# Performance work log

Hardware: AMD Instinct MI355X
Metric: run time of the kernel (lower is better)

## Reference

```python
import jax, jax.numpy as jnp
import numpy as np

BS, T, SIDE, H, Z, NSPK = 2048, 34, 30, 128, 16, 1024


def _lrelu(x):
    # nn.LeakyReLU(True) -> negative_slope=1.0, i.e. identity (faithful to source)
    return x


def _gru_cell(x, h, wih, whh, bih, bhh):
    # PyTorch GRU cell, gate order (r, z, n)
    gi = x @ wih.T + bih
    gh = h @ whh.T + bhh
    ir, iz, inn = jnp.split(gi, 3, axis=-1)
    hr, hz, hn = jnp.split(gh, 3, axis=-1)
    r = jax.nn.sigmoid(ir + hr)
    z = jax.nn.sigmoid(iz + hz)
    n = jnp.tanh(inn + r * hn)
    return (1.0 - z) * n + z * h


def setup_inputs() -> dict:
    key = jax.random.key(0)
    ks = iter(jax.random.split(key, 64))
    rn = lambda shape, s=0.05: jax.random.normal(next(ks), shape, jnp.float32) * s
    inp = {}
    inp["pre_seq"] = jax.random.normal(next(ks), (BS, T, 28), jnp.float32)
    inp["beats"] = jax.random.normal(next(ks), (BS, 2, T * SIDE), jnp.float32)
    inp["in_text"] = jnp.zeros((BS, T), jnp.int32)   # unused by forward
    inp["in_audio"] = jnp.zeros((BS, 1), jnp.float32)  # unused by forward
    inp["vid_indices"] = jax.random.randint(next(ks), (BS,), 0, NSPK)
    inp["eps"] = jax.random.normal(next(ks), (BS, Z), jnp.float32)  # reparameterize noise
    # speaker embedding net
    inp["spk_table"] = rn((NSPK, Z))
    inp["spk_lin_w"] = rn((Z, Z)); inp["spk_lin_b"] = jnp.zeros((Z,))
    inp["mu_w"] = rn((Z, Z)); inp["mu_b"] = jnp.zeros((Z,))
    inp["lv_w"] = rn((Z, Z)); inp["lv_b"] = jnp.zeros((Z,))
    # per-step MLPs
    inp["squ_w"] = rn((H, 3 * SIDE)); inp["squ_b"] = jnp.zeros((H,))
    inp["oenv_w"] = rn((H, 3 * SIDE)); inp["oenv_b"] = jnp.zeros((H,))
    inp["pose_w"] = rn((16, 28)); inp["pose_b"] = jnp.zeros((16,))
    inp["out_w"] = rn((H, H + 16)); inp["out_b"] = jnp.zeros((H,))
    inp["bo_w1"] = rn((64, H)); inp["bo_b1"] = jnp.zeros((64,))
    inp["bo_w2"] = rn((27, 64)); inp["bo_b2"] = jnp.zeros((27,))
    # GRU: 4 layers, bidirectional, hidden 128; layer0 input 144, layers1-3 input 256
    inp["w_ih_l0"] = rn((2, 3 * H, H + 16)); inp["w_hh_l0"] = rn((2, 3 * H, H))
    inp["b_ih_l0"] = jnp.zeros((2, 3 * H)); inp["b_hh_l0"] = jnp.zeros((2, 3 * H))
    inp["w_ih"] = rn((3, 2, 3 * H, 2 * H)); inp["w_hh"] = rn((3, 2, 3 * H, H))
    inp["b_ih"] = jnp.zeros((3, 2, 3 * H)); inp["b_hh"] = jnp.zeros((3, 2, 3 * H))
    return inp


def reference(pre_seq, beats, in_text, in_audio, vid_indices, eps,
              spk_table, spk_lin_w, spk_lin_b, mu_w, mu_b, lv_w, lv_b,
              squ_w, squ_b, oenv_w, oenv_b, pose_w, pose_b,
              out_w, out_b, bo_w1, bo_b1, bo_w2, bo_b2,
              w_ih_l0, w_hh_l0, b_ih_l0, b_hh_l0, w_ih, w_hh, b_ih, b_hh):
    bs = beats.shape[0]
    # speaker latent
    zc0 = spk_table[vid_indices] @ spk_lin_w.T + spk_lin_b
    z_mu = zc0 @ mu_w.T + mu_b
    z_logvar = zc0 @ lv_w.T + lv_b
    z_context = z_mu + eps * jnp.exp(0.5 * z_logvar)  # reparameterize

    # sub_beats windows: pad side_size zeros on each end, window=90, stride=30
    padded = jnp.pad(beats, ((0, 0), (0, 0), (SIDE, SIDE)))
    widx = SIDE * jnp.arange(T)[:, None] + jnp.arange(3 * SIDE)[None, :]
    win = padded[:, :, widx]  # (bs, 2, T, 90)

    # batch the tiny per-step MLPs across all 34 steps at once
    squ = _lrelu(jnp.einsum('bts,os->bto', win[:, 0], squ_w) + squ_b)
    oenv = _lrelu(jnp.einsum('bts,os->bto', win[:, 1], oenv_w) + oenv_b)
    sum_out = squ + oenv                                   # (bs, T, 128)
    pose = _lrelu(jnp.einsum('bts,os->bto', pre_seq, pose_w) + pose_b)  # (bs, T, 16)
    xs = jnp.concatenate([pose, sum_out], axis=-1).transpose(1, 0, 2)   # (T, bs, 144)

    def step(h, x):
        # h: (8, bs, H) = [l0_fwd, l0_bwd, l1_fwd, ...]; seq_len==1 per step
        hs = []
        for l in range(4):
            if l == 0:
                wi, wh, bi, bh = w_ih_l0, w_hh_l0, b_ih_l0, b_hh_l0
            else:
                wi, wh, bi, bh = w_ih[l - 1], w_hh[l - 1], b_ih[l - 1], b_hh[l - 1]
            hf = _gru_cell(x, h[2 * l], wi[0], wh[0], bi[0], bh[0])
            hb = _gru_cell(x, h[2 * l + 1], wi[1], wh[1], bi[1], bh[1])
            hs += [hf, hb]
            x = jnp.concatenate([hf, hb], axis=-1)
        # output = fwd half + bwd half of top layer
        return jnp.stack(hs), hs[-2] + hs[-1]

    h0 = jnp.zeros((8, bs, H), xs.dtype)  # decoder_hidden = None -> zeros
    _, outs = jax.lax.scan(step, h0, xs)  # (T, bs, H)

    zb = jnp.broadcast_to(z_context, (T,) + z_context.shape)  # (T, bs, 16)
    feat = _lrelu(jnp.concatenate([outs, zb], axis=-1) @ out_w.T + out_b)  # (T, bs, 128)
    beat = _lrelu(feat @ bo_w1.T + bo_b1) @ bo_w2.T + bo_b2               # (T, bs, 27)
    return beat.transpose(1, 0, 2), z_context, z_mu, z_logvar
```

## Files before the change

kernel.cpp:

```cpp
#include <hip/hip_runtime.h>
#include <hip/hip_bf16.h>
#include <stdint.h>

typedef __attribute__((ext_vector_type(8))) short bfrag;
typedef __attribute__((ext_vector_type(4))) float f32x4;

__device__ __forceinline__ unsigned short f2bf(float f){
  union { float f; unsigned u; } v; v.f = f;
  unsigned r = v.u + 0x7FFFu + ((v.u >> 16) & 1u);
  return (unsigned short)(r >> 16);
}
__device__ __forceinline__ f32x4 mfma16(bfrag a, bfrag b, f32x4 c){
  return __builtin_amdgcn_mfma_f32_16x16x32_bf16(a, b, c, 0, 0, 0);
}
__device__ __forceinline__ bfrag cvt8(const float* s){
  bfrag r;
  #pragma unroll
  for (int j = 0; j < 8; ++j) r[j] = (short)f2bf(s[j]);
  return r;
}

__global__ void k_pad(const float* __restrict__ beats, unsigned short* __restrict__ pad,
                      int NG){
  int g = blockIdx.x * 256 + threadIdx.x;
  if (g >= NG) return;
  int i8 = (g % 135) * 8;
  long rc = g / 135;
  const float* src = beats + rc * 1020;
  union { unsigned short u[8]; bfrag s; } o;
  #pragma unroll
  for (int j = 0; j < 8; ++j){
    int i = i8 + j;
    float v = (i >= 30 && i < 1050) ? src[i - 30] : 0.f;
    o.u[j] = f2bf(v);
  }
  *(bfrag*)(pad + rc * 1080 + i8) = o.s;
}

__global__ void k_prep(const float* __restrict__ squ_w, const float* __restrict__ oenv_w,
                       const float* __restrict__ pose_w, const float* __restrict__ out_w,
                       const float* __restrict__ bo_w1, const float* __restrict__ bo_w2,
                       unsigned short* __restrict__ B2w, unsigned short* __restrict__ posewp,
                       unsigned short* __restrict__ B1, unsigned short* __restrict__ bow1p,
                       unsigned short* __restrict__ bow2p){
  int i = blockIdx.x * 256 + threadIdx.x;
  if (i < 24576){
    int o = i / 192, k = i - o * 192;
    float v = 0.f;
    if (k < 90) v = squ_w[o * 90 + k];
    else if (k >= 96 && k < 186) v = oenv_w[o * 90 + (k - 96)];
    B2w[i] = f2bf(v);
    return;
  }
  i -= 24576;
  if (i < 512){
    int o = i / 32, k = i - o * 32;
    posewp[i] = f2bf(k < 28 ? pose_w[o * 28 + k] : 0.f);
    return;
  }
  i -= 512;
  if (i < 36864){
    int o = i / 288, k = i - o * 288;
    float v = 0.f;
    if (k < 128) v = out_w[o * 144 + k];
    else if (k < 256) v = out_w[o * 144 + (k - 128)];
    else if (k < 272) v = out_w[o * 144 + 128 + (k - 256)];
    B1[i] = f2bf(v);
    return;
  }
  i -= 36864;
  if (i < 8192){ bow1p[i] = f2bf(bo_w1[i]); return; }
  i -= 8192;
  if (i < 2048){
    int o = i / 64, k = i - o * 64;
    bow2p[i] = f2bf(o < 27 ? bo_w2[o * 64 + k] : 0.f);
  }
}

__global__ void k_z(const int* __restrict__ vid, const float* __restrict__ eps,
                    const float* __restrict__ spk_table, const float* __restrict__ slw,
                    const float* __restrict__ slb, const float* __restrict__ muw,
                    const float* __restrict__ mub, const float* __restrict__ lvw,
                    const float* __restrict__ lvb,
                    float* __restrict__ outp, unsigned short* __restrict__ zws){
  int b = blockIdx.x * 256 + threadIdx.x;
  if (b >= 2048) return;
  const float* tr = spk_table + (long)vid[b] * 16;
  float t[16], zc0[16];
  #pragma unroll
  for (int k = 0; k < 16; ++k) t[k] = tr[k];
  #pragma unroll
  for (int j = 0; j < 16; ++j){
    float a = slb[j];
    #pragma unroll
    for (int k = 0; k < 16; ++k) a += t[k] * slw[j * 16 + k];
    zc0[j] = a;
  }
  const long ZC = 1880064, ZMU = 1912832, ZLV = 1945600;
  #pragma unroll
  for (int j = 0; j < 16; ++j){
    float mu = mub[j], lv = lvb[j];
    #pragma unroll
    for (int k = 0; k < 16; ++k){ mu += zc0[k] * muw[j * 16 + k]; lv += zc0[k] * lvw[j * 16 + k]; }
    float zc = mu + eps[b * 16 + j] * __expf(0.5f * lv);
    outp[ZMU + b * 16 + j] = mu;
    outp[ZLV + b * 16 + j] = lv;
    outp[ZC + b * 16 + j] = zc;
    zws[b * 16 + j] = f2bf(zc);
  }
}

__global__ __launch_bounds__(256) void k_x0(
    const unsigned short* __restrict__ pad, const float* __restrict__ pre_seq,
    const unsigned short* __restrict__ B2w, const unsigned short* __restrict__ posewp,
    const float* __restrict__ squ_b, const float* __restrict__ oenv_b,
    const float* __restrict__ pose_b, unsigned short* __restrict__ xbuf0){
  int bid = blockIdx.x;
  int t = bid % 34, bt = bid / 34;
  int w = threadIdx.x >> 6, lane = threadIdx.x & 63;
  int q = lane >> 4, l15 = lane & 15;
  int row = bt * 64 + w * 16 + l15;
  bfrag a[6];
  {
    const unsigned short* p0 = pad + ((long)row * 2) * 1080 + 30 * t;
    #pragma unroll
    for (int kt = 0; kt < 6; ++kt){
      int k = kt * 32 + q * 8;
      const unsigned short* src = (k < 96) ? (p0 + k) : (p0 + 1080 + (k - 96));
      const unsigned int* pu = (const unsigned int*)src;
      union { unsigned int u[4]; bfrag s; } v;
      v.u[0] = pu[0]; v.u[1] = pu[1]; v.u[2] = pu[2]; v.u[3] = pu[3];
      a[kt] = v.s;
    }
  }
  f32x4 acc[8];
  #pragma unroll
  for (int nt = 0; nt < 8; ++nt) acc[nt] = (f32x4){0.f, 0.f, 0.f, 0.f};
  #pragma unroll
  for (int kt = 0; kt < 6; ++kt)
    #pragma unroll
    for (int nt = 0; nt < 8; ++nt){
      bfrag bf = *(const bfrag*)(B2w + ((nt * 16 + l15) * 192 + kt * 32 + q * 8));
      acc[nt] = mfma16(a[kt], bf, acc[nt]);
    }
  f32x4 accp = (f32x4){0.f, 0.f, 0.f, 0.f};
  {
    float av[8];
    const float* ps = pre_seq + ((long)row * 34 + t) * 28;
    if (q < 3){
      #pragma unroll
      for (int j = 0; j < 8; ++j) av[j] = ps[q * 8 + j];
    } else {
      #pragma unroll
      for (int j = 0; j < 4; ++j){ av[j] = ps[24 + j]; av[4 + j] = 0.f; }
    }
    bfrag ap = cvt8(av);
    bfrag bp = *(const bfrag*)(posewp + (l15 * 32 + q * 8));
    accp = mfma16(ap, bp, accp);
  }
  float pb = pose_b[l15];
  int rowc = bt * 64 + w * 16 + q * 4;
  #pragma unroll
  for (int r = 0; r < 4; ++r){
    long base = ((long)(rowc + r) * 34 + t) * 160;
    xbuf0[base + l15] = f2bf(accp[r] + pb);
    xbuf0[base + 144 + l15] = 0;
  }
  #pragma unroll
  for (int nt = 0; nt < 8; ++nt){
    int c = nt * 16 + l15;
    float sb = squ_b[c] + oenv_b[c];
    #pragma unroll
    for (int r = 0; r < 4; ++r){
      long base = ((long)(rowc + r) * 34 + t) * 160;
      xbuf0[base + 16 + c] = f2bf(acc[nt][r] + sb);
    }
  }
}

template<int KIT, int KI>
__global__ __launch_bounds__(512, 2) void k_gru(
    const unsigned short* __restrict__ xin, unsigned short* __restrict__ xout,
    const float* __restrict__ wih, const float* __restrict__ whh,
    const float* __restrict__ bih, const float* __restrict__ bhh, int WK){
  __shared__ unsigned short whh_lds[384 * 136];
  __shared__ unsigned short x_lds[2][16 * (KI + 8)];
  __shared__ unsigned short h_lds[2][16 * 136];
  int d = blockIdx.x & 1, bt = blockIdx.x >> 1;
  int tid = threadIdx.x;
  int w = tid >> 6, lane = tid & 63, q = lane >> 4, l15 = lane & 15;
  const float* wihd = wih + (long)d * 384 * WK;
  const float* whhd = whh + (long)d * 384 * 128;
  int col = w * 16 + l15;
  float bi0 = bih[d * 384 + col], bi1 = bih[d * 384 + 128 + col], bi2 = bih[d * 384 + 256 + col];
  float bh0 = bhh[d * 384 + col], bh1 = bhh[d * 384 + 128 + col], bh2 = bhh[d * 384 + 256 + col];
  for (int i = tid * 4; i < 384 * 128; i += 512 * 4){
    int n = i >> 7, k = i & 127;
    const float* s = whhd + i;
    unsigned short* dp = whh_lds + n * 136 + k;
    dp[0] = f2bf(s[0]); dp[1] = f2bf(s[1]); dp[2] = f2bf(s[2]); dp[3] = f2bf(s[3]);
  }
  bfrag bgi[3][KIT];
  #pragma unroll
  for (int g = 0; g < 3; ++g)
    #pragma unroll
    for (int kt = 0; kt < KIT; ++kt){
      int k = kt * 32 + q * 8;
      if (k < WK){
        float tmp[8];
        const float* s = wihd + (long)(g * 128 + col) * WK + k;
        #pragma unroll
        for (int j = 0; j < 8; ++j) tmp[j] = s[j];
        bgi[g][kt] = cvt8(tmp);
      } else {
        bgi[g][kt] = (bfrag){0, 0, 0, 0, 0, 0, 0, 0};
      }
    }
  const int NV = KI / 8;
  int xrow = tid / NV, xv = tid - xrow * NV;
  bool xact = (tid < 16 * NV);
  const unsigned short* xin_row = xin + ((long)(bt * 16 + (xact ? xrow : 0))) * 34 * KI;
  if (xact){
    bfrag v = *(const bfrag*)(xin_row + xv * 8);
    *(bfrag*)(&x_lds[0][xrow * (KI + 8) + xv * 8]) = v;
  }
  for (int i = tid; i < 16 * 136; i += 512){ h_lds[0][i] = 0; h_lds[1][i] = 0; }
  __syncthreads();

  f32x4 h_old = (f32x4){0.f, 0.f, 0.f, 0.f};
  int rowc = bt * 16 + q * 4;
  for (int t = 0; t < 34; ++t){
    int p = t & 1;
    bfrag xpf = (bfrag){0, 0, 0, 0, 0, 0, 0, 0};
    if (xact && t + 1 < 34)
      xpf = *(const bfrag*)(xin_row + (long)(t + 1) * KI + xv * 8);
    f32x4 gi0 = {0,0,0,0}, gi1 = {0,0,0,0}, gi2 = {0,0,0,0};
    f32x4 gh0 = {0,0,0,0}, gh1 = {0,0,0,0}, gh2 = {0,0,0,0};
    #pragma unroll
    for (int kt = 0; kt < KIT; ++kt){
      bfrag xa = *(const bfrag*)(&x_lds[p][l15 * (KI + 8) + kt * 32 + q * 8]);
      gi0 = mfma16(xa, bgi[0][kt], gi0);
      gi1 = mfma16(xa, bgi[1][kt], gi1);
      gi2 = mfma16(xa, bgi[2][kt], gi2);
    }
    #pragma unroll
    for (int kt = 0; kt < 4; ++kt){
      bfrag ha = *(const bfrag*)(&h_lds[p][l15 * 136 + kt * 32 + q * 8]);
      int ko = kt * 32 + q * 8;
      bfrag w0 = *(const bfrag*)(&whh_lds[(0 * 128 + col) * 136 + ko]);
      bfrag w1 = *(const bfrag*)(&whh_lds[(1 * 128 + col) * 136 + ko]);
      bfrag w2 = *(const bfrag*)(&whh_lds[(2 * 128 + col) * 136 + ko]);
      gh0 = mfma16(ha, w0, gh0);
      gh1 = mfma16(ha, w1, gh1);
      gh2 = mfma16(ha, w2, gh2);
    }
    f32x4 h_new;
    unsigned short hbf[4];
    #pragma unroll
    for (int r = 0; r < 4; ++r){
      float ir = gi0[r] + bi0, iz = gi1[r] + bi1, inn = gi2[r] + bi2;
      float hr = gh0[r] + bh0, hz = gh1[r] + bh1, hn = gh2[r] + bh2;
      float rg = 1.f / (1.f + __expf(-(ir + hr)));
      float zg = 1.f / (1.f + __expf(-(iz + hz)));
      float pre = inn + rg * hn;
      float ax = fabsf(pre);
      float th = 1.f - 2.f / (__expf(2.f * ax) + 1.f);
      th = (pre < 0.f) ? -th : th;
      float hv = (1.f - zg) * th + zg * h_old[r];
      h_new[r] = hv;
      hbf[r] = f2bf(hv);
    }
    h_old = h_new;
    #pragma unroll
    for (int r = 0; r < 4; ++r){
      h_lds[1 - p][(q * 4 + r) * 136 + col] = hbf[r];
      xout[((long)(rowc + r) * 34 + t) * 256 + d * 128 + col] = hbf[r];
    }
    if (xact && t + 1 < 34)
      *(bfrag*)(&x_lds[1 - p][xrow * (KI + 8) + xv * 8]) = xpf;
    __syncthreads();
  }
}

__global__ __launch_bounds__(512) void k_head(
    const unsigned short* __restrict__ xb, const unsigned short* __restrict__ zloc,
    const unsigned short* __restrict__ B1p, const unsigned short* __restrict__ bow1p,
    const unsigned short* __restrict__ bow2p,
    const float* __restrict__ out_b, const float* __restrict__ bo_b1,
    const float* __restrict__ bo_b2, float* __restrict__ outp){
  __shared__ unsigned short B1_lds[128 * 296];
  __shared__ unsigned short feat_lds[128 * 136];
  __shared__ unsigned short bt1_lds[128 * 72];
  int tid = threadIdx.x, w = tid >> 6, lane = tid & 63, q = lane >> 4, l15 = lane & 15;
  long rbase = (long)blockIdx.x * 128;
  for (int v = tid; v < 128 * 36; v += 512){
    int n = v / 36, kc = (v - n * 36) * 8;
    *(bfrag*)(&B1_lds[n * 296 + kc]) = *(const bfrag*)(B1p + n * 288 + kc);
  }
  __syncthreads();
  int rloc = w * 16 + l15;
  long rt = rbase + rloc;
  int bidx = (int)(rt / 34);
  bfrag a1[9];
  #pragma unroll
  for (int kt = 0; kt < 8; ++kt)
    a1[kt] = *(const bfrag*)(xb + rt * 256 + kt * 32 + q * 8);
  if (q < 2) a1[8] = *(const bfrag*)(zloc + (long)bidx * 16 + q * 8);
  else       a1[8] = (bfrag){0, 0, 0, 0, 0, 0, 0, 0};
  f32x4 acc[8];
  #pragma unroll
  for (int nt = 0; nt < 8; ++nt) acc[nt] = (f32x4){0.f, 0.f, 0.f, 0.f};
  #pragma unroll
  for (int kt = 0; kt < 9; ++kt)
    #pragma unroll
    for (int nt = 0; nt < 8; ++nt){
      bfrag b = *(const bfrag*)(&B1_lds[(nt * 16 + l15) * 296 + kt * 32 + q * 8]);
      acc[nt] = mfma16(a1[kt], b, acc[nt]);
    }
  #pragma unroll
  for (int nt = 0; nt < 8; ++nt){
    float bb = out_b[nt * 16 + l15];
    #pragma unroll
    for (int r = 0; r < 4; ++r)
      feat_lds[(w * 16 + q * 4 + r) * 136 + nt * 16 + l15] = f2bf(acc[nt][r] + bb);
  }
  __syncthreads();
  bfrag a2[4];
  #pragma unroll
  for (int kt = 0; kt < 4; ++kt)
    a2[kt] = *(const bfrag*)(&feat_lds[rloc * 136 + kt * 32 + q * 8]);
  f32x4 acc2[4];
  #pragma unroll
  for (int nt = 0; nt < 4; ++nt) acc2[nt] = (f32x4){0.f, 0.f, 0.f, 0.f};
  #pragma unroll
  for (int kt = 0; kt < 4; ++kt)
    #pragma unroll
    for (int nt = 0; nt < 4; ++nt){
      bfrag b = *(const bfrag*)(bow1p + ((nt * 16 + l15) * 128 + kt * 32 + q * 8));
      acc2[nt] = mfma16(a2[kt], b, acc2[nt]);
    }
  #pragma unroll
  for (int nt = 0; nt < 4; ++nt){
    float bb = bo_b1[nt * 16 + l15];
    #pragma unroll
    for (int r = 0; r < 4; ++r)
      bt1_lds[(w * 16 + q * 4 + r) * 72 + nt * 16 + l15] = f2bf(acc2[nt][r] + bb);
  }
  __syncthreads();
  bfrag a3[2];
  #pragma unroll
  for (int kt = 0; kt < 2; ++kt)
    a3[kt] = *(const bfrag*)(&bt1_lds[rloc * 72 + kt * 32 + q * 8]);
  f32x4 acc3[2];
  #pragma unroll
  for (int nt = 0; nt < 2; ++nt) acc3[nt] = (f32x4){0.f, 0.f, 0.f, 0.f};
  #pragma unroll
  for (int kt = 0; kt < 2; ++kt)
    #pragma unroll
    for (int nt = 0; nt < 2; ++nt){
      bfrag b = *(const bfrag*)(bow2p + ((nt * 16 + l15) * 64 + kt * 32 + q * 8));
      acc3[nt] = mfma16(a3[kt], b, acc3[nt]);
    }
  #pragma unroll
  for (int nt = 0; nt < 2; ++nt){
    int n = nt * 16 + l15;
    if (n < 27){
      float bb = bo_b2[n];
      #pragma unroll
      for (int r = 0; r < 4; ++r){
        long rowg = rbase + w * 16 + q * 4 + r;
        outp[rowg * 27 + n] = acc3[nt][r] + bb;
      }
    }
  }
}

extern "C" void kernel_launch(void* const* d_in, const int* in_sizes, int n_in,
                              void* d_out, int out_size, void* d_ws, size_t ws_size,
                              hipStream_t stream){
  (void)in_sizes; (void)n_in; (void)out_size;
  const float* pre_seq = (const float*)d_in[0];
  const float* beats   = (const float*)d_in[1];
  const int*   vid     = (const int*)d_in[4];
  const float* eps     = (const float*)d_in[5];
  const float* spk_table = (const float*)d_in[6];
  const float* slw = (const float*)d_in[7];
  const float* slb = (const float*)d_in[8];
  const float* muw = (const float*)d_in[9];
  const float* mub = (const float*)d_in[10];
  const float* lvw = (const float*)d_in[11];
  const float* lvb = (const float*)d_in[12];
  const float* squ_w = (const float*)d_in[13];
  const float* squ_b = (const float*)d_in[14];
  const float* oenv_w = (const float*)d_in[15];
  const float* oenv_b = (const float*)d_in[16];
  const float* pose_w = (const float*)d_in[17];
  const float* pose_b = (const float*)d_in[18];
  const float* out_w = (const float*)d_in[19];
  const float* out_b = (const float*)d_in[20];
  const float* bo_w1 = (const float*)d_in[21];
  const float* bo_b1 = (const float*)d_in[22];
  const float* bo_w2 = (const float*)d_in[23];
  const float* bo_b2 = (const float*)d_in[24];
  const float* w_ih_l0 = (const float*)d_in[25];
  const float* w_hh_l0 = (const float*)d_in[26];
  const float* b_ih_l0 = (const float*)d_in[27];
  const float* b_hh_l0 = (const float*)d_in[28];
  const float* w_ih = (const float*)d_in[29];
  const float* w_hh = (const float*)d_in[30];
  const float* b_ih = (const float*)d_in[31];
  const float* b_hh = (const float*)d_in[32];
  float* outp = (float*)d_out;
  unsigned short* ws = (unsigned short*)d_ws;

  const long o_z     = 0;
  const long o_B2w   = 32768;
  const long o_posew = o_B2w + 24576;
  const long o_B1    = o_posew + 512;
  const long o_bw1   = o_B1 + 36864;
  const long o_bw2   = o_bw1 + 8192;
  const long o_chunk = o_bw2 + 2048;

  int Bc;
  {
    const size_t margin = 1u << 20;
    size_t need2048 = (size_t)(o_chunk + 2048L * 25008) * 2 + margin;
    size_t need512  = (size_t)(o_chunk + 512L  * 25008) * 2 + margin;
    if      (ws_size >= need2048) Bc = 2048;
    else if (ws_size >= need512)  Bc = 512;
    else                          Bc = 128;
  }
  const int C = 2048 / Bc;
  const long o_pad = o_chunk;
  const long o_x0  = o_pad + (long)Bc * 2160;
  const long o_A   = o_x0  + (long)Bc * 5440;
  const long o_B   = o_A   + (long)Bc * 8704;

  k_prep<<<282, 256, 0, stream>>>(squ_w, oenv_w, pose_w, out_w, bo_w1, bo_w2,
                                  ws + o_B2w, ws + o_posew, ws + o_B1, ws + o_bw1, ws + o_bw2);
  k_z<<<8, 256, 0, stream>>>(vid, eps, spk_table, slw, slb, muw, mub, lvw, lvb, outp, ws + o_z);

  for (int c = 0; c < C; ++c){
    long b0 = (long)c * Bc;
    int NG = Bc * 270;
    k_pad<<<NG / 256, 256, 0, stream>>>(beats + b0 * 2040, ws + o_pad, NG);
    k_x0<<<34 * (Bc / 64), 256, 0, stream>>>(ws + o_pad, pre_seq + b0 * 952,
                                             ws + o_B2w, ws + o_posew,
                                             squ_b, oenv_b, pose_b, ws + o_x0);
    k_gru<5, 160><<<Bc / 8, 512, 0, stream>>>(ws + o_x0, ws + o_A,
                                              w_ih_l0, w_hh_l0, b_ih_l0, b_hh_l0, 144);
    k_gru<8, 256><<<Bc / 8, 512, 0, stream>>>(ws + o_A, ws + o_B,
                                              w_ih, w_hh, b_ih, b_hh, 256);
    k_gru<8, 256><<<Bc / 8, 512, 0, stream>>>(ws + o_B, ws + o_A,
                                              w_ih + 1L * 2 * 384 * 256, w_hh + 1L * 2 * 384 * 128,
                                              b_ih + 2 * 384, b_hh + 2 * 384, 256);
    k_gru<8, 256><<<Bc / 8, 512, 0, stream>>>(ws + o_A, ws + o_B,
                                              w_ih + 2L * 2 * 384 * 256, w_hh + 2L * 2 * 384 * 128,
                                              b_ih + 4 * 384, b_hh + 4 * 384, 256);
    k_head<<<Bc * 34 / 128, 512, 0, stream>>>(ws + o_B, ws + o_z,
                                              ws + o_B1, ws + o_bw1, ws + o_bw2,
                                              out_b, bo_b1, bo_b2, outp + b0 * 918);
  }
}
```

Before: 533.2 us.

## Hold GRU recurrent weights in registers and pipeline next-step input projection

The recurrent weight matrix moves from LDS into per-lane register fragments, which removes three LDS reads per k-tile on every timestep. The input projection for step t+1 is now computed after h is written, off the recurrence critical path, using a triple-buffered x tile with a prefetch distance of two. Global stores of h are deferred by one step. The cost is much higher register pressure (bgi plus 12 bwh fragments), which risks spills under launch_bounds(512,2).

```diff
diff --git a/kernel.cpp b/kernel.cpp
--- a/kernel.cpp
+++ b/kernel.cpp
@@ -183,8 +183,7 @@
     const unsigned short* __restrict__ xin, unsigned short* __restrict__ xout,
     const float* __restrict__ wih, const float* __restrict__ whh,
     const float* __restrict__ bih, const float* __restrict__ bhh, int WK){
-  __shared__ unsigned short whh_lds[384 * 136];
-  __shared__ unsigned short x_lds[2][16 * (KI + 8)];
+  __shared__ unsigned short x_lds[3][16 * (KI + 8)];
   __shared__ unsigned short h_lds[2][16 * 136];
   int d = blockIdx.x & 1, bt = blockIdx.x >> 1;
   int tid = threadIdx.x;
@@ -194,12 +193,6 @@
   int col = w * 16 + l15;
   float bi0 = bih[d * 384 + col], bi1 = bih[d * 384 + 128 + col], bi2 = bih[d * 384 + 256 + col];
   float bh0 = bhh[d * 384 + col], bh1 = bhh[d * 384 + 128 + col], bh2 = bhh[d * 384 + 256 + col];
-  for (int i = tid * 4; i < 384 * 128; i += 512 * 4){
-    int n = i >> 7, k = i & 127;
-    const float* s = whhd + i;
-    unsigned short* dp = whh_lds + n * 136 + k;
-    dp[0] = f2bf(s[0]); dp[1] = f2bf(s[1]); dp[2] = f2bf(s[2]); dp[3] = f2bf(s[3]);
-  }
   bfrag bgi[3][KIT];
   #pragma unroll
   for (int g = 0; g < 3; ++g)
@@ -216,49 +209,62 @@
         bgi[g][kt] = (bfrag){0, 0, 0, 0, 0, 0, 0, 0};
       }
     }
+  bfrag bwh[3][4];
+  #pragma unroll
+  for (int g = 0; g < 3; ++g)
+    #pragma unroll
+    for (int kt = 0; kt < 4; ++kt){
+      float tmp[8];
+      const float* s = whhd + (long)(g * 128 + col) * 128 + kt * 32 + q * 8;
+      #pragma unroll
+      for (int j = 0; j < 8; ++j) tmp[j] = s[j];
+      bwh[g][kt] = cvt8(tmp);
+    }
   const int NV = KI / 8;
   int xrow = tid / NV, xv = tid - xrow * NV;
   bool xact = (tid < 16 * NV);
   const unsigned short* xin_row = xin + ((long)(bt * 16 + (xact ? xrow : 0))) * 34 * KI;
   if (xact){
-    bfrag v = *(const bfrag*)(xin_row + xv * 8);
-    *(bfrag*)(&x_lds[0][xrow * (KI + 8) + xv * 8]) = v;
-  }
-  for (int i = tid; i < 16 * 136; i += 512){ h_lds[0][i] = 0; h_lds[1][i] = 0; }
+    *(bfrag*)(&x_lds[0][xrow * (KI + 8) + xv * 8]) = *(const bfrag*)(xin_row + xv * 8);
+    *(bfrag*)(&x_lds[1][xrow * (KI + 8) + xv * 8]) = *(const bfrag*)(xin_row + (long)KI + xv * 8);
+  }
+  for (int i = tid; i < 16 * 136; i += 512) h_lds[0][i] = 0;
   __syncthreads();
 
-  f32x4 h_old = (f32x4){0.f, 0.f, 0.f, 0.f};
+  f32x4 gc0 = {0,0,0,0}, gc1 = {0,0,0,0}, gc2 = {0,0,0,0};
+  #pragma unroll
+  for (int kt = 0; kt < KIT; ++kt){
+    bfrag xa = *(const bfrag*)(&x_lds[0][l15 * (KI + 8) + kt * 32 + q * 8]);
+    gc0 = mfma16(xa, bgi[0][kt], gc0);
+    gc1 = mfma16(xa, bgi[1][kt], gc1);
+    gc2 = mfma16(xa, bgi[2][kt], gc2);
+  }
+  bfrag xpf = (bfrag){0, 0, 0, 0, 0, 0, 0, 0};
+  if (xact) xpf = *(const bfrag*)(xin_row + 2L * KI + xv * 8);
+
+  f32x4 h_old = {0,0,0,0};
+  unsigned short hbf[4] = {0, 0, 0, 0};
   int rowc = bt * 16 + q * 4;
+  int p = 0;
+  int s1 = 1, s2 = 2;
   for (int t = 0; t < 34; ++t){
-    int p = t & 1;
-    bfrag xpf = (bfrag){0, 0, 0, 0, 0, 0, 0, 0};
-    if (xact && t + 1 < 34)
-      xpf = *(const bfrag*)(xin_row + (long)(t + 1) * KI + xv * 8);
-    f32x4 gi0 = {0,0,0,0}, gi1 = {0,0,0,0}, gi2 = {0,0,0,0};
+    if (t > 0){
+      #pragma unroll
+      for (int r = 0; r < 4; ++r)
+        xout[((long)(rowc + r) * 34 + (t - 1)) * 256 + d * 128 + col] = hbf[r];
+    }
     f32x4 gh0 = {0,0,0,0}, gh1 = {0,0,0,0}, gh2 = {0,0,0,0};
-    #pragma unroll
-    for (int kt = 0; kt < KIT; ++kt){
-      bfrag xa = *(const bfrag*)(&x_lds[p][l15 * (KI + 8) + kt * 32 + q * 8]);
-      gi0 = mfma16(xa, bgi[0][kt], gi0);
-      gi1 = mfma16(xa, bgi[1][kt], gi1);
-      gi2 = mfma16(xa, bgi[2][kt], gi2);
-    }
     #pragma unroll
     for (int kt = 0; kt < 4; ++kt){
       bfrag ha = *(const bfrag*)(&h_lds[p][l15 * 136 + kt * 32 + q * 8]);
-      int ko = kt * 32 + q * 8;
-      bfrag w0 = *(const bfrag*)(&whh_lds[(0 * 128 + col) * 136 + ko]);
-      bfrag w1 = *(const bfrag*)(&whh_lds[(1 * 128 + col) * 136 + ko]);
-      bfrag w2 = *(const bfrag*)(&whh_lds[(2 * 128 + col) * 136 + ko]);
-      gh0 = mfma16(ha, w0, gh0);
-      gh1 = mfma16(ha, w1, gh1);
-      gh2 = mfma16(ha, w2, gh2);
+      gh0 = mfma16(ha, bwh[0][kt], gh0);
+      gh1 = mfma16(ha, bwh[1][kt], gh1);
+      gh2 = mfma16(ha, bwh[2][kt], gh2);
     }
     f32x4 h_new;
-    unsigned short hbf[4];
     #pragma unroll
     for (int r = 0; r < 4; ++r){
-      float ir = gi0[r] + bi0, iz = gi1[r] + bi1, inn = gi2[r] + bi2;
+      float ir = gc0[r] + bi0, iz = gc1[r] + bi1, inn = gc2[r] + bi2;
       float hr = gh0[r] + bh0, hz = gh1[r] + bh1, hn = gh2[r] + bh2;
       float rg = 1.f / (1.f + __expf(-(ir + hr)));
       float zg = 1.f / (1.f + __expf(-(iz + hz)));
@@ -272,14 +278,31 @@
     }
     h_old = h_new;
     #pragma unroll
-    for (int r = 0; r < 4; ++r){
+    for (int r = 0; r < 4; ++r)
       h_lds[1 - p][(q * 4 + r) * 136 + col] = hbf[r];
-      xout[((long)(rowc + r) * 34 + t) * 256 + d * 128 + col] = hbf[r];
-    }
-    if (xact && t + 1 < 34)
-      *(bfrag*)(&x_lds[1 - p][xrow * (KI + 8) + xv * 8]) = xpf;
+    if (t + 1 < 34){
+      f32x4 gn0 = {0,0,0,0}, gn1 = {0,0,0,0}, gn2 = {0,0,0,0};
+      #pragma unroll
+      for (int kt = 0; kt < KIT; ++kt){
+        bfrag xa = *(const bfrag*)(&x_lds[s1][l15 * (KI + 8) + kt * 32 + q * 8]);
+        gn0 = mfma16(xa, bgi[0][kt], gn0);
+        gn1 = mfma16(xa, bgi[1][kt], gn1);
+        gn2 = mfma16(xa, bgi[2][kt], gn2);
+      }
+      gc0 = gn0; gc1 = gn1; gc2 = gn2;
+    }
+    if (xact && t + 2 < 34){
+      *(bfrag*)(&x_lds[s2][xrow * (KI + 8) + xv * 8]) = xpf;
+      if (t + 3 < 34) xpf = *(const bfrag*)(xin_row + (long)(t + 3) * KI + xv * 8);
+    }
+    s1 = (s1 == 2) ? 0 : s1 + 1;
+    s2 = (s2 == 2) ? 0 : s2 + 1;
+    p ^= 1;
     __syncthreads();
   }
+  #pragma unroll
+  for (int r = 0; r < 4; ++r)
+    xout[((long)(rowc + r) * 34 + 33) * 256 + d * 128 + col] = hbf[r];
 }
 
 __global__ __launch_bounds__(512) void k_head(
```

Result: faster. 499.1 us (-6.4%).
